# Performance work log

Measured on AMD Instinct MI355X. Metric: run time of the kernel, lower is better.

Reference implementation:

```python
import jax, jax.numpy as jnp
import numpy as np

N_NODES = 100000
N_EDGES = 1600000
D_FEAT = 256
HIDDEN = 256
OUT = 128


def _glorot(key, shape):
    fan_in, fan_out = shape[1], shape[0]
    lim = float(np.sqrt(6.0 / (fan_in + fan_out)))
    return jax.random.uniform(key, shape, jnp.float32, -lim, lim)


def setup_inputs() -> dict:
    key = jax.random.key(0)
    ks = jax.random.split(key, 12)
    x = jax.random.normal(ks[0], (N_NODES, D_FEAT), jnp.float32)
    edge_index = jax.random.randint(ks[1], (2, N_EDGES), 0, N_NODES, jnp.int64)
    return {
        "x": x,
        "edge_index": edge_index,
        # SAGEConv1: lin_l (neighbors, has bias), lin_r (root, no bias)
        "W1l": _glorot(ks[2], (HIDDEN, D_FEAT)),
        "b1l": jnp.zeros((HIDDEN,), jnp.float32),
        "W1r": _glorot(ks[3], (HIDDEN, D_FEAT)),
        # SAGEConv2
        "W2l": _glorot(ks[4], (OUT, HIDDEN)),
        "b2l": jnp.zeros((OUT,), jnp.float32),
        "W2r": _glorot(ks[5], (OUT, HIDDEN)),
        # EdgeDecoder
        "Wd1": _glorot(ks[6], (OUT, 2 * OUT)),
        "bd1": jnp.zeros((OUT,), jnp.float32),
        "Wd2": _glorot(ks[7], (1, OUT)),
        "bd2": jnp.zeros((1,), jnp.float32),
    }


def _sage_conv(x, src, dst, Wl, bl, Wr):
    # mean-aggregate source features into destination nodes (PyG SAGEConv, aggr='mean')
    msg_sum = jax.ops.segment_sum(x[src], dst, num_segments=N_NODES)  # [N, d]
    cnt = jax.ops.segment_sum(jnp.ones((src.shape[0],), x.dtype), dst, num_segments=N_NODES)
    mean = msg_sum / jnp.maximum(cnt, 1.0)[:, None]
    return mean @ Wl.T + bl + x @ Wr.T


def reference(x, edge_index, W1l, b1l, W1r, W2l, b2l, W2r, Wd1, bd1, Wd2, bd2):
    src, dst = edge_index[0], edge_index[1]
    # NodeEncoder
    h = jax.nn.relu(_sage_conv(x, src, dst, W1l, b1l, W1r))
    z = _sage_conv(h, src, dst, W2l, b2l, W2r)  # [N, OUT]
    # EdgeDecoder: gather per-edge endpoint embeddings, concat, MLP
    zc = jnp.concatenate([z[src], z[dst]], axis=-1)  # [E, 2*OUT]
    hd = jax.nn.relu(zc @ Wd1.T + bd1)
    out = hd @ Wd2.T + bd2  # [E, 1]
    return out.reshape(-1)
```

## Files before the change

kernel.cpp:

```cpp
#include <hip/hip_runtime.h>
#include <stdint.h>

static constexpr int NN = 100000;
static constexpr int NE = 1600000;
static constexpr int NB_SCAN = (NN + 255) / 256;
static constexpr int NB_CVTX = NN * 256 / 4 / 256;
static constexpr int NB_HIST = NE / 256;
static constexpr int NB_CVTW = 897;

typedef __bf16 bf16;
typedef __bf16 bf16x4 __attribute__((ext_vector_type(4)));
typedef __bf16 bf16x8 __attribute__((ext_vector_type(8)));
typedef float floatx4 __attribute__((ext_vector_type(4)));

__device__ __forceinline__ void async16(const void* g, void* l) {
  __builtin_amdgcn_global_load_lds(
      (const __attribute__((address_space(1))) void*)g,
      (__attribute__((address_space(3))) void*)l, 16, 0, 0);
}

__device__ __forceinline__ uint32_t pk4_fp8(float a, float b, float c, float d) {
  uint32_t v = 0;
  v = (uint32_t)__builtin_amdgcn_cvt_pk_fp8_f32(a, b, (int)v, false);
  v = (uint32_t)__builtin_amdgcn_cvt_pk_fp8_f32(c, d, (int)v, true);
  return v;
}

__device__ __forceinline__ void acc_fp8x8(float* a, uint2 v) {
  a[0] += __builtin_amdgcn_cvt_f32_fp8(v.x, 0);
  a[1] += __builtin_amdgcn_cvt_f32_fp8(v.x, 1);
  a[2] += __builtin_amdgcn_cvt_f32_fp8(v.x, 2);
  a[3] += __builtin_amdgcn_cvt_f32_fp8(v.x, 3);
  a[4] += __builtin_amdgcn_cvt_f32_fp8(v.y, 0);
  a[5] += __builtin_amdgcn_cvt_f32_fp8(v.y, 1);
  a[6] += __builtin_amdgcn_cvt_f32_fp8(v.y, 2);
  a[7] += __builtin_amdgcn_cvt_f32_fp8(v.y, 3);
}

__device__ __forceinline__ int clampN(int c) {
  return ((unsigned)c < (unsigned)NN) ? c : 0;
}

__global__ void k_cvtx_hist(const float* __restrict__ x, bf16* __restrict__ xb,
                            uint32_t* __restrict__ xq,
                            const int* __restrict__ dst, int* __restrict__ cnt8,
                            uint16_t* __restrict__ rank) {
  int b = blockIdx.x;
  int m = b % 5;
  if (m < 4) {
    int cb = (b / 5) * 4 + m;
    int t = cb * 256 + threadIdx.x;
    const float4 v = ((const float4*)x)[t];
    bf16x4 o;
    o.x = (bf16)v.x; o.y = (bf16)v.y; o.z = (bf16)v.z; o.w = (bf16)v.w;
    ((bf16x4*)xb)[t] = o;
    xq[t] = pk4_fp8(v.x, v.y, v.z, v.w);
  } else {
    int hb = b / 5;
    int e = hb * 256 + threadIdx.x;
    uint32_t xcd;
    asm("s_getreg_b32 %0, hwreg(HW_REG_XCC_ID)" : "=s"(xcd));
    xcd &= 7u;
    int d = dst[e];
    int old = __hip_atomic_fetch_add(&cnt8[(size_t)xcd * NN + d], 1,
                                     __ATOMIC_RELAXED, __HIP_MEMORY_SCOPE_WORKGROUP);
    rank[e] = (uint16_t)((xcd << 12) | ((uint32_t)old & 0xFFFu));
  }
}

__global__ void k_cvtw_scanpart(
    const float* __restrict__ W1l, const float* __restrict__ W1r,
    const float* __restrict__ W2l, const float* __restrict__ W2r,
    const float* __restrict__ Wd1, const float* __restrict__ bd1,
    bf16* __restrict__ B1, bf16* __restrict__ B2,
    bf16* __restrict__ Bd, float* __restrict__ biasPQ,
    const int* __restrict__ cnt8, int* __restrict__ part, int N) {
  int b = blockIdx.x;
  if (b < NB_CVTW) {
    int g = b * 256 + threadIdx.x;
    if (g < 131072) {
      int o = g >> 9, k = g & 511;
      float v = (k < 256) ? W1l[o * 256 + k] : W1r[o * 256 + k - 256];
      B1[g] = (bf16)v;
    } else if (g < 131072 + 65536) {
      int t = g - 131072;
      int o = t >> 8, k = t & 255;
      float v = (o < 128) ? W2l[o * 256 + k] : W2r[(o - 128) * 256 + k];
      B2[t] = (bf16)v;
    } else if (g < 131072 + 65536 + 32768) {
      int t = g - 196608;
      int o = t >> 7, k = t & 127;
      float v = (o < 128) ? Wd1[o * 256 + k] : Wd1[(o - 128) * 256 + 128 + k];
      Bd[t] = (bf16)v;
    } else if (g < 131072 + 65536 + 32768 + 256) {
      int t = g - 229376;
      biasPQ[t] = (t < 128) ? bd1[t] : 0.0f;
    }
  } else {
    __shared__ int sh[256];
    int bb = b - NB_CVTW;
    int t = threadIdx.x;
    int i = bb * 256 + t;
    int tot = 0;
    if (i < N) {
#pragma unroll
      for (int xx = 0; xx < 8; ++xx) tot += cnt8[(size_t)xx * NN + i];
    }
    sh[t] = tot;
    __syncthreads();
    for (int off = 128; off > 0; off >>= 1) {
      if (t < off) sh[t] += sh[t + off];
      __syncthreads();
    }
    if (t == 0) part[bb] = sh[0];
  }
}

__global__ __launch_bounds__(512) void k_scan_mid(int* __restrict__ part, int NB) {
  __shared__ int sh[512];
  int t = threadIdx.x;
  int v = (t < NB) ? part[t] : 0;
  sh[t] = v;
  __syncthreads();
  for (int off = 1; off < 512; off <<= 1) {
    int u = (t >= off) ? sh[t - off] : 0;
    __syncthreads();
    sh[t] += u;
    __syncthreads();
  }
  if (t < NB) part[t] = sh[t] - v;
}

__global__ void k_scan_fin(int* __restrict__ cnt8, const int* __restrict__ part,
                           int* __restrict__ rowptr, int N, int E) {
  __shared__ int sh[256];
  int t = threadIdx.x;
  int i = blockIdx.x * 256 + t;
  int c[8];
  int v = 0;
  if (i < N) {
#pragma unroll
    for (int xx = 0; xx < 8; ++xx) { c[xx] = cnt8[(size_t)xx * NN + i]; v += c[xx]; }
  } else {
#pragma unroll
    for (int xx = 0; xx < 8; ++xx) c[xx] = 0;
  }
  sh[t] = v;
  __syncthreads();
  for (int off = 1; off < 256; off <<= 1) {
    int u = (t >= off) ? sh[t - off] : 0;
    __syncthreads();
    sh[t] += u;
    __syncthreads();
  }
  if (i < N) {
    int base = part[blockIdx.x] + sh[t] - v;
    rowptr[i] = base;
#pragma unroll
    for (int xx = 0; xx < 8; ++xx) { cnt8[(size_t)xx * NN + i] = base; base += c[xx]; }
  }
  if (i == 0) rowptr[N] = E;
}

__global__ void k_fill(const int* __restrict__ src, const int* __restrict__ dst,
                       const int* __restrict__ rptr8,
                       const uint16_t* __restrict__ rank,
                       int* __restrict__ csr, int E) {
  int e = blockIdx.x * 256 + threadIdx.x;
  if (e < E) {
    int d = dst[e];
    uint32_t rv = rank[e];
    int pos = rptr8[(size_t)(rv >> 12) * NN + d] + (int)(rv & 0xFFFu);
    if ((unsigned)pos >= (unsigned)E) pos = 0;
    csr[pos] = src[e];
  }
}

__global__ void k_agg(const uint8_t* __restrict__ xq, const int* __restrict__ rowptr,
                      const int* __restrict__ csr, bf16* __restrict__ mean) {
  int wave = threadIdx.x >> 6, lane = threadIdx.x & 63;
  int n = blockIdx.x * 4 + wave;
  int s = rowptr[n], e = rowptr[n + 1];
  int half = lane >> 5, l32 = lane & 31;
  float a[8] = {};
  const uint8_t* base = xq + l32 * 8;
  int i = s + half;
  for (; i + 6 < e; i += 8) {
    int c0 = clampN(csr[i]), c1 = clampN(csr[i + 2]);
    int c2 = clampN(csr[i + 4]), c3 = clampN(csr[i + 6]);
    uint2 v0 = *(const uint2*)(base + (size_t)c0 * 256);
    uint2 v1 = *(const uint2*)(base + (size_t)c1 * 256);
    uint2 v2 = *(const uint2*)(base + (size_t)c2 * 256);
    uint2 v3 = *(const uint2*)(base + (size_t)c3 * 256);
    acc_fp8x8(a, v0); acc_fp8x8(a, v1); acc_fp8x8(a, v2); acc_fp8x8(a, v3);
  }
  for (; i < e; i += 2) {
    uint2 v = *(const uint2*)(base + (size_t)clampN(csr[i]) * 256);
    acc_fp8x8(a, v);
  }
  int deg = e - s;
  float sc = 1.0f / (float)(deg > 0 ? deg : 1);
  bf16x8 o;
#pragma unroll
  for (int j = 0; j < 8; ++j) {
    float t = a[j] + __shfl_xor(a[j], 32);
    o[j] = (bf16)(t * sc);
  }
  if (half == 0)
    *(bf16x8*)(mean + (size_t)n * 256 + l32 * 8) = o;
}

__global__ void k_agg2z(const uint8_t* __restrict__ hq, const bf16* __restrict__ hr,
                        const int* __restrict__ rowptr, const int* __restrict__ csr,
                        const float* __restrict__ b2l, bf16* __restrict__ zf) {
  int wave = threadIdx.x >> 6, lane = threadIdx.x & 63;
  int n = blockIdx.x * 4 + wave;
  int s = rowptr[n], e = rowptr[n + 1];
  int sub = lane >> 4, l16 = lane & 15;
  float a[8] = {};
  const uint8_t* base = hq + l16 * 8;
  int i = s + sub;
  for (; i + 4 < e; i += 8) {
    int c0 = clampN(csr[i]), c1 = clampN(csr[i + 4]);
    uint2 v0 = *(const uint2*)(base + (size_t)c0 * 128);
    uint2 v1 = *(const uint2*)(base + (size_t)c1 * 128);
    acc_fp8x8(a, v0); acc_fp8x8(a, v1);
  }
  for (; i < e; i += 4) {
    uint2 v = *(const uint2*)(base + (size_t)clampN(csr[i]) * 128);
    acc_fp8x8(a, v);
  }
  int deg = e - s;
  float sc = 1.0f / (float)(deg > 0 ? deg : 1);
  bf16x8 hv = *(const bf16x8*)(hr + (size_t)n * 128 + l16 * 8);
  const float4* b4 = (const float4*)(b2l + l16 * 8);
  float4 ba = b4[0], bb = b4[1];
  float bl[8] = {ba.x, ba.y, ba.z, ba.w, bb.x, bb.y, bb.z, bb.w};
  bf16x8 o;
#pragma unroll
  for (int j = 0; j < 8; ++j) {
    float t = a[j];
    t += __shfl_xor(t, 16);
    t += __shfl_xor(t, 32);
    o[j] = (bf16)(t * sc + (float)hv[j] + bl[j]);
  }
  if (sub == 0)
    *(bf16x8*)(zf + (size_t)n * 128 + l16 * 8) = o;
}

__global__ __launch_bounds__(512) void k_fused12(
    const bf16* __restrict__ A1, const bf16* __restrict__ A2,
    const bf16* __restrict__ B1, const float* __restrict__ b1l,
    const bf16* __restrict__ B2, uint8_t* __restrict__ hq,
    bf16* __restrict__ hr, int Nrows) {
  __shared__ bf16 Hs[128 * 256];
  __shared__ bf16 As[128 * 64];
  __shared__ bf16 Bs[256 * 64];
  const int tid = threadIdx.x, wave = tid >> 6, lane = tid & 63;
  const int quad = lane >> 4, l16 = lane & 15;
  const int rowBase = blockIdx.x * 128;
  const int wr = (wave >> 2) * 64;
  const int wc = (wave & 3) * 64;
  floatx4 acc[4][4] = {};

  for (int kc = 0; kc < 8; ++kc) {
    const bf16* Asrc = (kc < 4) ? A1 : A2;
    const int kb = (kc & 3) * 64;
    for (int i = 0; i < 2; ++i) {
      int u = wave * 128 + i * 64 + lane;
      int row = u >> 3, seg = u & 7;
      int sg = seg ^ (row & 7);
      int node = rowBase + row;
      if (node >= Nrows) node = Nrows - 1;
      async16(Asrc + (size_t)node * 256 + kb + sg * 8, &As[(wave * 128 + i * 64) * 8]);
    }
    for (int i = 0; i < 4; ++i) {
      int u = wave * 256 + i * 64 + lane;
      int row = u >> 3, seg = u & 7;
      int sg = seg ^ (row & 7);
      async16(B1 + (size_t)row * 512 + kc * 64 + sg * 8, &Bs[(wave * 256 + i * 64) * 8]);
    }
    __syncthreads();
    for (int ks = 0; ks < 2; ++ks) {
      bf16x8 af[4], bq[4];
      const int sw = (ks * 4 + quad) ^ (l16 & 7);
      for (int mt = 0; mt < 4; ++mt)
        af[mt] = *(const bf16x8*)&As[(wr + mt * 16 + l16) * 64 + sw * 8];
      for (int nt = 0; nt < 4; ++nt)
        bq[nt] = *(const bf16x8*)&Bs[(wc + nt * 16 + l16) * 64 + sw * 8];
      for (int mt = 0; mt < 4; ++mt)
        for (int nt = 0; nt < 4; ++nt)
          acc[mt][nt] = __builtin_amdgcn_mfma_f32_16x16x32_bf16(af[mt], bq[nt], acc[mt][nt], 0, 0, 0);
    }
    __syncthreads();
  }

  {
    float bv1[4];
    for (int nt = 0; nt < 4; ++nt) bv1[nt] = b1l[wc + nt * 16 + l16];
    for (int mt = 0; mt < 4; ++mt)
      for (int nt = 0; nt < 4; ++nt) {
        int col = wc + nt * 16 + l16;
        int c = col >> 3;
        for (int r = 0; r < 4; ++r) {
          int row = wr + mt * 16 + quad * 4 + r;
          float v = fmaxf(acc[mt][nt][r] + bv1[nt], 0.0f);
          Hs[row * 256 + (c ^ (row & 7)) * 8 + (col & 7)] = (bf16)v;
          acc[mt][nt][r] = 0.0f;
        }
      }
  }
  __syncthreads();

  for (int kc = 0; kc < 4; ++kc) {
    for (int i = 0; i < 4; ++i) {
      int u = wave * 256 + i * 64 + lane;
      int row = u >> 3, seg = u & 7;
      int sg = seg ^ (row & 7);
      async16(B2 + (size_t)row * 256 + kc * 64 + sg * 8, &Bs[(wave * 256 + i * 64) * 8]);
    }
    __syncthreads();
    for (int ks = 0; ks < 2; ++ks) {
      bf16x8 af[4], bq[4];
      const int swb = (ks * 4 + quad) ^ (l16 & 7);
      const int ck = kc * 8 + ks * 4 + quad;
      for (int mt = 0; mt < 4; ++mt) {
        int row = wr + mt * 16 + l16;
        af[mt] = *(const bf16x8*)&Hs[row * 256 + (ck ^ (row & 7)) * 8];
      }
      for (int nt = 0; nt < 4; ++nt)
        bq[nt] = *(const bf16x8*)&Bs[(wc + nt * 16 + l16) * 64 + swb * 8];
      for (int mt = 0; mt < 4; ++mt)
        for (int nt = 0; nt < 4; ++nt)
          acc[mt][nt] = __builtin_amdgcn_mfma_f32_16x16x32_bf16(af[mt], bq[nt], acc[mt][nt], 0, 0, 0);
    }
    __syncthreads();
  }

  for (int mt = 0; mt < 4; ++mt)
    for (int nt = 0; nt < 4; ++nt) {
      int oc = wc + nt * 16 + l16;
      for (int r = 0; r < 4; ++r) {
        int grow = rowBase + wr + mt * 16 + quad * 4 + r;
        if (grow < Nrows) {
          float v = acc[mt][nt][r];
          if (oc < 128) {
            uint32_t pk = (uint32_t)__builtin_amdgcn_cvt_pk_fp8_f32(v, v, 0, false);
            hq[(size_t)grow * 128 + oc] = (uint8_t)pk;
          } else {
            hr[(size_t)grow * 128 + oc - 128] = (bf16)v;
          }
        }
      }
    }
}

template <int KDIM, int EPI>
__global__ __launch_bounds__(256) void k_gemm(
    const bf16* __restrict__ A, const bf16* __restrict__ B,
    const float* __restrict__ bias, void* __restrict__ out1,
    void* __restrict__ out2, int Nrows) {
  __shared__ bf16 As[128 * 64];
  __shared__ bf16 Bs[128 * 64];
  const int tid = threadIdx.x, wave = tid >> 6, lane = tid & 63;
  const int quad = lane >> 4, l16 = lane & 15;
  const int rowBase = blockIdx.y * 128;
  const int colBase = blockIdx.x * 128;
  const int wr = (wave >> 1) * 64;
  const int wc = (wave & 1) * 64;
  floatx4 acc[4][4] = {};

  for (int kc = 0; kc < KDIM / 64; ++kc) {
    for (int i = 0; i < 4; ++i) {
      int u = wave * 256 + i * 64 + lane;
      int row = u >> 3, seg = u & 7;
      int sg = seg ^ (row & 7);
      int node = rowBase + row;
      if (node >= Nrows) node = Nrows - 1;
      async16(A + (size_t)node * KDIM + kc * 64 + sg * 8, &As[(wave * 256 + i * 64) * 8]);
    }
    for (int i = 0; i < 4; ++i) {
      int u = wave * 256 + i * 64 + lane;
      int row = u >> 3, seg = u & 7;
      int sg = seg ^ (row & 7);
      async16(B + (size_t)(colBase + row) * KDIM + kc * 64 + sg * 8,
              &Bs[(wave * 256 + i * 64) * 8]);
    }
    __syncthreads();
    for (int ks = 0; ks < 2; ++ks) {
      bf16x8 af[4], bq[4];
      const int sw = (ks * 4 + quad) ^ (l16 & 7);
      for (int mt = 0; mt < 4; ++mt)
        af[mt] = *(const bf16x8*)&As[(wr + mt * 16 + l16) * 64 + sw * 8];
      for (int nt = 0; nt < 4; ++nt)
        bq[nt] = *(const bf16x8*)&Bs[(wc + nt * 16 + l16) * 64 + sw * 8];
      for (int mt = 0; mt < 4; ++mt)
        for (int nt = 0; nt < 4; ++nt)
          acc[mt][nt] = __builtin_amdgcn_mfma_f32_16x16x32_bf16(af[mt], bq[nt], acc[mt][nt], 0, 0, 0);
    }
    __syncthreads();
  }
  float bv[4];
  for (int nt = 0; nt < 4; ++nt)
    bv[nt] = (EPI == 2) ? bias[colBase + wc + nt * 16 + l16] : 0.0f;
  const bool lowHalf = (colBase == 0);
  for (int mt = 0; mt < 4; ++mt)
    for (int nt = 0; nt < 4; ++nt) {
      int gcol = colBase + wc + nt * 16 + l16;
      for (int r = 0; r < 4; ++r) {
        int grow = rowBase + wr + mt * 16 + quad * 4 + r;
        if (grow < Nrows) {
          float v = acc[mt][nt][r] + bv[nt];
          if (lowHalf) {
            if (EPI == 1) {
              uint32_t pk = (uint32_t)__builtin_amdgcn_cvt_pk_fp8_f32(v, v, 0, false);
              ((uint8_t*)out1)[(size_t)grow * 128 + gcol] = (uint8_t)pk;
            } else {
              ((bf16*)out1)[(size_t)grow * 128 + gcol] = (bf16)v;
            }
          } else {
            ((bf16*)out2)[(size_t)grow * 128 + gcol - 128] = (bf16)v;
          }
        }
      }
    }
}

__global__ __launch_bounds__(256) void k_edge(
    const bf16* __restrict__ P, const bf16* __restrict__ Q,
    const int* __restrict__ rowptr, const int* __restrict__ csr,
    const float* __restrict__ wd2, const float* __restrict__ bd2,
    float* __restrict__ outCSR) {
  int wave = threadIdx.x >> 6, lane = threadIdx.x & 63;
  int n = blockIdx.x * 4 + wave;
  int s = rowptr[n], e = rowptr[n + 1];
  int sub = lane >> 4, l16 = lane & 15;
  bf16x8 qv = *(const bf16x8*)(Q + (size_t)n * 128 + l16 * 8);
  float qf[8];
#pragma unroll
  for (int j = 0; j < 8; ++j) qf[j] = (float)qv[j];
  const float4* w4 = (const float4*)(wd2 + l16 * 8);
  float4 wa = w4[0], wb = w4[1];
  float w[8] = {wa.x, wa.y, wa.z, wa.w, wb.x, wb.y, wb.z, wb.w};
  const float bout = bd2[0];
  int i = s + sub;
  for (; i + 4 < e; i += 8) {
    int c0 = clampN(csr[i]), c1 = clampN(csr[i + 4]);
    bf16x8 p0 = *(const bf16x8*)(P + (size_t)c0 * 128 + l16 * 8);
    bf16x8 p1 = *(const bf16x8*)(P + (size_t)c1 * 128 + l16 * 8);
    float a0 = 0.f, a1 = 0.f;
#pragma unroll
    for (int j = 0; j < 8; ++j) {
      a0 += fmaxf((float)p0[j] + qf[j], 0.f) * w[j];
      a1 += fmaxf((float)p1[j] + qf[j], 0.f) * w[j];
    }
    a0 += __shfl_xor(a0, 1); a1 += __shfl_xor(a1, 1);
    a0 += __shfl_xor(a0, 2); a1 += __shfl_xor(a1, 2);
    a0 += __shfl_xor(a0, 4); a1 += __shfl_xor(a1, 4);
    a0 += __shfl_xor(a0, 8); a1 += __shfl_xor(a1, 8);
    if (l16 == 0) { outCSR[i] = a0 + bout; outCSR[i + 4] = a1 + bout; }
  }
  for (; i < e; i += 4) {
    int c = clampN(csr[i]);
    bf16x8 p = *(const bf16x8*)(P + (size_t)c * 128 + l16 * 8);
    float a = 0.f;
#pragma unroll
    for (int j = 0; j < 8; ++j)
      a += fmaxf((float)p[j] + qf[j], 0.f) * w[j];
    a += __shfl_xor(a, 1);
    a += __shfl_xor(a, 2);
    a += __shfl_xor(a, 4);
    a += __shfl_xor(a, 8);
    if (l16 == 0) outCSR[i] = a + bout;
  }
}

__global__ void k_perm(const int* __restrict__ dst, const uint16_t* __restrict__ rank,
                       const int* __restrict__ rptr8, const float* __restrict__ outCSR,
                       float* __restrict__ out, int E) {
  int e = blockIdx.x * 256 + threadIdx.x;
  if (e < E) {
    int d = dst[e];
    uint32_t rv = rank[e];
    int pos = rptr8[(size_t)(rv >> 12) * NN + d] + (int)(rv & 0xFFFu);
    if ((unsigned)pos >= (unsigned)E) pos = 0;
    out[e] = outCSR[pos];
  }
}

extern "C" void kernel_launch(void* const* d_in, const int* in_sizes, int n_in,
                              void* d_out, int out_size, void* d_ws, size_t ws_size,
                              hipStream_t stream) {
  const float* x   = (const float*)d_in[0];
  const int*   ei  = (const int*)d_in[1];
  const float* W1l = (const float*)d_in[2];
  const float* b1l = (const float*)d_in[3];
  const float* W1r = (const float*)d_in[4];
  const float* W2l = (const float*)d_in[5];
  const float* b2l = (const float*)d_in[6];
  const float* W2r = (const float*)d_in[7];
  const float* Wd1 = (const float*)d_in[8];
  const float* bd1 = (const float*)d_in[9];
  const float* Wd2 = (const float*)d_in[10];
  const float* bd2 = (const float*)d_in[11];
  float* out = (float*)d_out;

  const int N = NN, E = NE;
  const int* srcv = ei;
  const int* dstv = ei + E;

  char* w = (char*)d_ws;
  size_t off = 0;
  auto take = [&](size_t bytes) {
    size_t o = off;
    off = (off + bytes + 255) & ~(size_t)255;
    return o;
  };
  int*      cnt8   = (int*)(w + take((size_t)8 * N * 4));
  int*      rowptr = (int*)(w + take((size_t)(N + 1) * 4));
  int*      part   = (int*)(w + take((size_t)NB_SCAN * 4));
  uint16_t* rank   = (uint16_t*)(w + take((size_t)E * 2));
  int*      csr    = (int*)(w + take((size_t)E * 4));
  bf16*     xb     = (bf16*)(w + take((size_t)N * 256 * 2));
  uint8_t*  xq     = (uint8_t*)(w + take((size_t)N * 256));
  bf16*     mean   = (bf16*)(w + take((size_t)N * 256 * 2));
  bf16*     h      = (bf16*)(w + take((size_t)N * 256 * 2));
  bf16*     zf     = (bf16*)(w + take((size_t)N * 128 * 2));
  bf16*     B1     = (bf16*)(w + take((size_t)131072 * 2));
  bf16*     B2     = (bf16*)(w + take((size_t)65536 * 2));
  bf16*     Bd     = (bf16*)(w + take((size_t)32768 * 2));
  float*    biasPQ = (float*)(w + take((size_t)256 * 4));
  int*     rptr8 = cnt8;
  float*   outCSR = (float*)xb;
  uint8_t* hq = (uint8_t*)h;
  bf16*    hr = (bf16*)(hq + (size_t)N * 128);
  bf16*    P  = mean;
  bf16*    Q  = mean + (size_t)N * 128;
  (void)ws_size; (void)n_in; (void)in_sizes; (void)out_size;

  hipMemsetAsync(cnt8, 0, (size_t)8 * N * 4, stream);

  k_cvtx_hist<<<NB_CVTX + NB_HIST, 256, 0, stream>>>(x, xb, (uint32_t*)xq, dstv, cnt8, rank);
  k_cvtw_scanpart<<<NB_CVTW + NB_SCAN, 256, 0, stream>>>(
      W1l, W1r, W2l, W2r, Wd1, bd1, B1, B2, Bd, biasPQ, cnt8, part, N);
  k_scan_mid<<<1, 512, 0, stream>>>(part, NB_SCAN);
  k_scan_fin<<<NB_SCAN, 256, 0, stream>>>(cnt8, part, rowptr, N, E);
  k_fill<<<E / 256, 256, 0, stream>>>(srcv, dstv, rptr8, rank, csr, E);

  k_agg<<<N / 4, 256, 0, stream>>>(xq, rowptr, csr, mean);
  k_fused12<<<782, 512, 0, stream>>>(mean, xb, B1, b1l, B2, hq, hr, N);
  k_agg2z<<<N / 4, 256, 0, stream>>>(hq, hr, rowptr, csr, b2l, zf);
  k_gemm<128, 2><<<dim3(2, 782), 256, 0, stream>>>(zf, Bd, biasPQ, P, Q, N);
  k_edge<<<N / 4, 256, 0, stream>>>(P, Q, rowptr, csr, Wd2, bd2, outCSR);
  k_perm<<<E / 256, 256, 0, stream>>>(dstv, rank, rptr8, outCSR, out, E);
}
```

Before: 570.8 us.

## Double-buffer LDS staging in fused two-layer GEMM to overlap loads with MFMA

Converts k_fused12's two GEMM phases into one 12-step software pipeline with ping-pong As/Bs shared buffers. The next K-chunk's async global-to-LDS loads are issued before computing the current chunk, and explicit vmcnt waits plus raw s_barrier replace the __syncthreads pairs. The goal is to hide global load latency behind MFMA work and drop a barrier per step. LDS use rises to the full 160KB, and the reliance on hand-counted vmcnt and bare barriers is fragile. The grid-size expression change leaves the value unchanged.

Measured after the change: 592.0 us. 1.04x slower.

```diff
diff --git a/kernel.cpp b/kernel.cpp
--- a/kernel.cpp
+++ b/kernel.cpp
@@ -254,8 +254,8 @@
     const bf16* __restrict__ B2, uint8_t* __restrict__ hq,
     bf16* __restrict__ hr, int Nrows) {
   __shared__ bf16 Hs[128 * 256];
-  __shared__ bf16 As[128 * 64];
-  __shared__ bf16 Bs[256 * 64];
+  __shared__ bf16 As[2][128 * 64];
+  __shared__ bf16 Bs[2][256 * 64];
   const int tid = threadIdx.x, wave = tid >> 6, lane = tid & 63;
   const int quad = lane >> 4, l16 = lane & 15;
   const int rowBase = blockIdx.x * 128;
@@ -263,78 +263,104 @@
   const int wc = (wave & 3) * 64;
   floatx4 acc[4][4] = {};
 
-  for (int kc = 0; kc < 8; ++kc) {
+  auto stageA = [&](int kc, bf16* dst) {
     const bf16* Asrc = (kc < 4) ? A1 : A2;
     const int kb = (kc & 3) * 64;
+#pragma unroll
     for (int i = 0; i < 2; ++i) {
       int u = wave * 128 + i * 64 + lane;
       int row = u >> 3, seg = u & 7;
       int sg = seg ^ (row & 7);
       int node = rowBase + row;
       if (node >= Nrows) node = Nrows - 1;
-      async16(Asrc + (size_t)node * 256 + kb + sg * 8, &As[(wave * 128 + i * 64) * 8]);
-    }
+      async16(Asrc + (size_t)node * 256 + kb + sg * 8, dst + (wave * 128 + i * 64) * 8);
+    }
+  };
+  auto stageB1 = [&](int kc, bf16* dst) {
+#pragma unroll
     for (int i = 0; i < 4; ++i) {
       int u = wave * 256 + i * 64 + lane;
       int row = u >> 3, seg = u & 7;
       int sg = seg ^ (row & 7);
-      async16(B1 + (size_t)row * 512 + kc * 64 + sg * 8, &Bs[(wave * 256 + i * 64) * 8]);
-    }
-    __syncthreads();
-    for (int ks = 0; ks < 2; ++ks) {
-      bf16x8 af[4], bq[4];
-      const int sw = (ks * 4 + quad) ^ (l16 & 7);
-      for (int mt = 0; mt < 4; ++mt)
-        af[mt] = *(const bf16x8*)&As[(wr + mt * 16 + l16) * 64 + sw * 8];
-      for (int nt = 0; nt < 4; ++nt)
-        bq[nt] = *(const bf16x8*)&Bs[(wc + nt * 16 + l16) * 64 + sw * 8];
-      for (int mt = 0; mt < 4; ++mt)
-        for (int nt = 0; nt < 4; ++nt)
-          acc[mt][nt] = __builtin_amdgcn_mfma_f32_16x16x32_bf16(af[mt], bq[nt], acc[mt][nt], 0, 0, 0);
-    }
-    __syncthreads();
-  }
-
-  {
-    float bv1[4];
-    for (int nt = 0; nt < 4; ++nt) bv1[nt] = b1l[wc + nt * 16 + l16];
-    for (int mt = 0; mt < 4; ++mt)
-      for (int nt = 0; nt < 4; ++nt) {
-        int col = wc + nt * 16 + l16;
-        int c = col >> 3;
-        for (int r = 0; r < 4; ++r) {
-          int row = wr + mt * 16 + quad * 4 + r;
-          float v = fmaxf(acc[mt][nt][r] + bv1[nt], 0.0f);
-          Hs[row * 256 + (c ^ (row & 7)) * 8 + (col & 7)] = (bf16)v;
-          acc[mt][nt][r] = 0.0f;
-        }
-      }
-  }
-  __syncthreads();
-
-  for (int kc = 0; kc < 4; ++kc) {
+      async16(B1 + (size_t)row * 512 + kc * 64 + sg * 8, dst + (wave * 256 + i * 64) * 8);
+    }
+  };
+  auto stageB2 = [&](int kc, bf16* dst) {
+#pragma unroll
     for (int i = 0; i < 4; ++i) {
       int u = wave * 256 + i * 64 + lane;
       int row = u >> 3, seg = u & 7;
       int sg = seg ^ (row & 7);
-      async16(B2 + (size_t)row * 256 + kc * 64 + sg * 8, &Bs[(wave * 256 + i * 64) * 8]);
-    }
-    __syncthreads();
-    for (int ks = 0; ks < 2; ++ks) {
-      bf16x8 af[4], bq[4];
-      const int swb = (ks * 4 + quad) ^ (l16 & 7);
-      const int ck = kc * 8 + ks * 4 + quad;
-      for (int mt = 0; mt < 4; ++mt) {
-        int row = wr + mt * 16 + l16;
-        af[mt] = *(const bf16x8*)&Hs[row * 256 + (ck ^ (row & 7)) * 8];
+      async16(B2 + (size_t)row * 256 + kc * 64 + sg * 8, dst + (wave * 256 + i * 64) * 8);
+    }
+  };
+
+  stageA(0, As[0]);
+  stageB1(0, Bs[0]);
+
+  for (int s = 0; s < 12; ++s) {
+    const int nb = s + 1;
+    if (nb < 8) {
+      stageA(nb, As[nb & 1]);
+      stageB1(nb, Bs[nb & 1]);
+      asm volatile("s_waitcnt vmcnt(6)" ::: "memory");
+    } else if (nb < 12) {
+      stageB2(nb - 8, Bs[nb & 1]);
+      asm volatile("s_waitcnt vmcnt(4)" ::: "memory");
+    } else {
+      asm volatile("s_waitcnt vmcnt(0)" ::: "memory");
+    }
+    __builtin_amdgcn_sched_barrier(0);
+    __builtin_amdgcn_s_barrier();
+
+    if (s < 8) {
+      const bf16* asb = As[s & 1];
+      const bf16* bsb = Bs[s & 1];
+      for (int ks = 0; ks < 2; ++ks) {
+        bf16x8 af[4], bq[4];
+        const int sw = (ks * 4 + quad) ^ (l16 & 7);
+        for (int mt = 0; mt < 4; ++mt)
+          af[mt] = *(const bf16x8*)&asb[(wr + mt * 16 + l16) * 64 + sw * 8];
+        for (int nt = 0; nt < 4; ++nt)
+          bq[nt] = *(const bf16x8*)&bsb[(wc + nt * 16 + l16) * 64 + sw * 8];
+        for (int mt = 0; mt < 4; ++mt)
+          for (int nt = 0; nt < 4; ++nt)
+            acc[mt][nt] = __builtin_amdgcn_mfma_f32_16x16x32_bf16(af[mt], bq[nt], acc[mt][nt], 0, 0, 0);
       }
-      for (int nt = 0; nt < 4; ++nt)
-        bq[nt] = *(const bf16x8*)&Bs[(wc + nt * 16 + l16) * 64 + swb * 8];
-      for (int mt = 0; mt < 4; ++mt)
+      if (s == 7) {
+        float bv1[4];
+        for (int nt = 0; nt < 4; ++nt) bv1[nt] = b1l[wc + nt * 16 + l16];
+        for (int mt = 0; mt < 4; ++mt)
+          for (int nt = 0; nt < 4; ++nt) {
+            int col = wc + nt * 16 + l16;
+            int c = col >> 3;
+            for (int r = 0; r < 4; ++r) {
+              int row = wr + mt * 16 + quad * 4 + r;
+              float v = fmaxf(acc[mt][nt][r] + bv1[nt], 0.0f);
+              Hs[row * 256 + (c ^ (row & 7)) * 8 + (col & 7)] = (bf16)v;
+              acc[mt][nt][r] = 0.0f;
+            }
+          }
+      }
+    } else {
+      const bf16* bsb = Bs[s & 1];
+      const int kc = s - 8;
+      for (int ks = 0; ks < 2; ++ks) {
+        bf16x8 af[4], bq[4];
+        const int swb = (ks * 4 + quad) ^ (l16 & 7);
+        const int ck = kc * 8 + ks * 4 + quad;
+        for (int mt = 0; mt < 4; ++mt) {
+          int row = wr + mt * 16 + l16;
+          af[mt] = *(const bf16x8*)&Hs[row * 256 + (ck ^ (row & 7)) * 8];
+        }
         for (int nt = 0; nt < 4; ++nt)
-          acc[mt][nt] = __builtin_amdgcn_mfma_f32_16x16x32_bf16(af[mt], bq[nt], acc[mt][nt], 0, 0, 0);
-    }
-    __syncthreads();
+          bq[nt] = *(const bf16x8*)&bsb[(wc + nt * 16 + l16) * 64 + swb * 8];
+        for (int mt = 0; mt < 4; ++mt)
+          for (int nt = 0; nt < 4; ++nt)
+            acc[mt][nt] = __builtin_amdgcn_mfma_f32_16x16x32_bf16(af[mt], bq[nt], acc[mt][nt], 0, 0, 0);
+      }
+    }
+    __builtin_amdgcn_s_barrier();
   }
 
   for (int mt = 0; mt < 4; ++mt)
@@ -548,7 +574,7 @@
   k_fill<<<E / 256, 256, 0, stream>>>(srcv, dstv, rptr8, rank, csr, E);
 
   k_agg<<<N / 4, 256, 0, stream>>>(xq, rowptr, csr, mean);
-  k_fused12<<<782, 512, 0, stream>>>(mean, xb, B1, b1l, B2, hq, hr, N);
+  k_fused12<<<(NN + 127) / 128, 512, 0, stream>>>(mean, xb, B1, b1l, B2, hq, hr, N);
   k_agg2z<<<N / 4, 256, 0, stream>>>(hq, hr, rowptr, csr, b2l, zf);
   k_gemm<128, 2><<<dim3(2, 782), 256, 0, stream>>>(zf, Bd, biasPQ, P, Q, N);
   k_edge<<<N / 4, 256, 0, stream>>>(P, Q, rowptr, csr, Wd2, bd2, outCSR);
```
